# Kernel optimization log

Measured on AMD Instinct MI355X. Metric: run time of the kernel, lower is better.

The kernel has to match this reference:

```python
import jax, jax.numpy as jnp
import numpy as np

H = 256  # hidden_channels
N_USERS = 100000
N_MOVIES = 50000
N_EDGES = 500000


def setup_inputs() -> dict:
    key = jax.random.key(0)
    k1, k2, k3, k4, k5, k6, k7 = jax.random.split(key, 7)
    user_emb = jax.random.normal(k1, (N_USERS, H), dtype=jnp.float32)
    movie_emb = jax.random.normal(k2, (N_MOVIES, H), dtype=jnp.float32)
    edge_label_index = jax.random.randint(k3, (2, N_EDGES), 0, N_MOVIES, dtype=jnp.int64)
    # Linear(2H, H) and Linear(H, 1) params, torch default init scale
    s1 = 1.0 / np.sqrt(2 * H)
    s2 = 1.0 / np.sqrt(H)
    W1 = jax.random.uniform(k4, (2 * H, H), dtype=jnp.float32, minval=-s1, maxval=s1)
    b1 = jax.random.uniform(k5, (H,), dtype=jnp.float32, minval=-s1, maxval=s1)
    W2 = jax.random.uniform(k6, (H, 1), dtype=jnp.float32, minval=-s2, maxval=s2)
    b2 = jax.random.uniform(k7, (1,), dtype=jnp.float32, minval=-s2, maxval=s2)
    return {"user_emb": user_emb, "movie_emb": movie_emb,
            "edge_label_index": edge_label_index,
            "W1": W1, "b1": b1, "W2": W2, "b2": b2}


def reference(user_emb, movie_emb, edge_label_index, W1, b1, W2, b2):
    u = user_emb[edge_label_index[0]]    # [E, H]
    m = movie_emb[edge_label_index[1]]   # [E, H]
    x = jnp.concatenate([u, m], axis=-1)  # [E, 2H]
    x = jax.nn.relu(x @ W1 + b1)          # [E, H]
    return x @ W2 + b2                    # [E, 1]
```

## Files before the change

kernel.cpp:

```cpp
#include <hip/hip_runtime.h>
#include <hip/hip_bf16.h>

typedef __attribute__((ext_vector_type(8))) short v8s;
typedef __attribute__((ext_vector_type(4))) float v4f;

constexpr int H  = 256;
constexpr int K2 = 512;
constexpr int XS = 72;
constexpr int WS = 72;

__device__ inline unsigned short f2bf(float f) {
    unsigned int u = __builtin_bit_cast(unsigned int, f);
    u += 0x7FFFu + ((u >> 16) & 1u);
    return (unsigned short)(u >> 16);
}
__device__ inline float bf2f(unsigned short s) {
    return __builtin_bit_cast(float, (unsigned int)s << 16);
}

__global__ void w1_transpose_kernel(const float* __restrict__ w1,
                                    unsigned short* __restrict__ w1t) {
    __shared__ float tile[32][33];
    const int bk = blockIdx.x;
    const int bn = blockIdx.y;
    const int tx = threadIdx.x & 31;
    const int ty8 = threadIdx.x >> 5;
#pragma unroll
    for (int i = 0; i < 4; ++i) {
        int ty = i * 8 + ty8;
        tile[ty][tx] = w1[(size_t)(bk * 32 + ty) * H + bn * 32 + tx];
    }
    __syncthreads();
#pragma unroll
    for (int i = 0; i < 4; ++i) {
        int ty = i * 8 + ty8;
        w1t[(size_t)(bn * 32 + ty) * K2 + bk * 32 + tx] = f2bf(tile[tx][ty]);
    }
}

__global__ __launch_bounds__(512, 4) void emb_gemm_fused_kernel(
    const float* __restrict__ user_emb,
    const float* __restrict__ movie_emb,
    const unsigned short* __restrict__ w1t,
    const float* __restrict__ b1,
    unsigned short* __restrict__ P,
    unsigned short* __restrict__ Q,
    const int n_users, const int n_movies, const int nbu)
{
    __shared__ unsigned short Xs[64 * XS];
    __shared__ unsigned short Wts[H * WS];

    const int  isMovie = (blockIdx.x >= nbu) ? 1 : 0;
    const float* emb  = isMovie ? movie_emb : user_emb;
    unsigned short* outp = isMovie ? Q : P;
    const int  M     = isMovie ? n_movies : n_users;
    const int  kofs  = isMovie ? 256 : 0;
    const long m0    = (long)(blockIdx.x - (isMovie ? nbu : 0)) * 64;

    const int t    = threadIdx.x;
    const int wave = t >> 6;
    const int lane = t & 63;
    const int wm   = wave >> 2;
    const int wn   = wave & 3;
    const int quad = lane >> 4;
    const int l16  = lane & 15;

    const int xr = t >> 3;
    const int xc = t & 7;
    long mr = m0 + xr; if (mr >= M) mr = M - 1;
    const float* arow = emb + (size_t)mr * H;

    const int wr  = t >> 3;
    const int wc8 = t & 7;
    const unsigned short* wbase = w1t + (size_t)wr * K2 + kofs + wc8 * 8;

    v4f acc[2][4];
#pragma unroll
    for (int mt = 0; mt < 2; ++mt)
#pragma unroll
        for (int nt = 0; nt < 4; ++nt)
            acc[mt][nt] = (v4f){0.f, 0.f, 0.f, 0.f};

    v4f a0 = *(const v4f*)(arow + xc * 8);
    v4f a1 = *(const v4f*)(arow + xc * 8 + 4);
    v8s wq[4];
#pragma unroll
    for (int j = 0; j < 4; ++j)
        wq[j] = *(const v8s*)(wbase + (size_t)j * 64 * K2);

    for (int kt = 0; kt < 4; ++kt) {
        __syncthreads();
        {
            v8s xv;
#pragma unroll
            for (int i = 0; i < 4; ++i) { xv[i] = (short)f2bf(a0[i]); xv[4+i] = (short)f2bf(a1[i]); }
            *(v8s*)(Xs + xr * XS + xc * 8) = xv;
        }
#pragma unroll
        for (int j = 0; j < 4; ++j)
            *(v8s*)(Wts + (j * 64 + wr) * WS + wc8 * 8) = wq[j];
        if (kt < 3) {
            const int kn = kt + 1;
            a0 = *(const v4f*)(arow + kn * 64 + xc * 8);
            a1 = *(const v4f*)(arow + kn * 64 + xc * 8 + 4);
#pragma unroll
            for (int j = 0; j < 4; ++j)
                wq[j] = *(const v8s*)(wbase + (size_t)j * 64 * K2 + kn * 64);
        }
        __syncthreads();
#pragma unroll
        for (int ks = 0; ks < 2; ++ks) {
            v8s af[2], bf[4];
#pragma unroll
            for (int mt = 0; mt < 2; ++mt)
                af[mt] = *(const v8s*)(Xs + (wm * 32 + mt * 16 + l16) * XS + ks * 32 + quad * 8);
#pragma unroll
            for (int nt = 0; nt < 4; ++nt)
                bf[nt] = *(const v8s*)(Wts + (wn * 64 + nt * 16 + l16) * WS + ks * 32 + quad * 8);
#pragma unroll
            for (int mt = 0; mt < 2; ++mt)
#pragma unroll
                for (int nt = 0; nt < 4; ++nt)
                    acc[mt][nt] = __builtin_amdgcn_mfma_f32_16x16x32_bf16(
                        af[mt], bf[nt], acc[mt][nt], 0, 0, 0);
        }
    }

    float bv[4];
#pragma unroll
    for (int nt = 0; nt < 4; ++nt)
        bv[nt] = isMovie ? 0.f : b1[wn * 64 + nt * 16 + l16];

#pragma unroll
    for (int mt = 0; mt < 2; ++mt) {
#pragma unroll
        for (int j = 0; j < 4; ++j) {
            long m = m0 + wm * 32 + mt * 16 + quad * 4 + j;
            if (m < M) {
#pragma unroll
                for (int nt = 0; nt < 4; ++nt) {
                    int n = wn * 64 + nt * 16 + l16;
                    outp[(size_t)m * H + n] = f2bf(acc[mt][nt][j] + bv[nt]);
                }
            }
        }
    }
}

__global__ __launch_bounds__(256, 8) void edge_score_kernel(
    const unsigned short* __restrict__ P,
    const unsigned short* __restrict__ Q,
    const int* __restrict__ eli,
    const float* __restrict__ w2,
    const float* __restrict__ b2,
    float* __restrict__ out,
    const int E, const int n_users, const int n_movies)
{
    const int t   = threadIdx.x;
    const int hw  = t >> 5;
    const int l32 = t & 31;

    float w2v[8];
    {
        v4f a = *(const v4f*)(w2 + l32 * 8);
        v4f b = *(const v4f*)(w2 + l32 * 8 + 4);
#pragma unroll
        for (int i = 0; i < 4; ++i) { w2v[i] = a[i]; w2v[4 + i] = b[i]; }
    }
    const float b2v = b2[0];
    const long base = (long)blockIdx.x * 64;

    int us[8], ms[8];
#pragma unroll
    for (int i = 0; i < 8; ++i) {
        long e = base + i * 8 + hw;
        long ec = (e < E) ? e : 0;
        int u = eli[ec];
        int m = eli[(long)E + ec];
        us[i] = u < 0 ? 0 : (u >= n_users  ? n_users  - 1 : u);
        ms[i] = m < 0 ? 0 : (m >= n_movies ? n_movies - 1 : m);
    }

    v8s pv = *(const v8s*)(P + (size_t)us[0] * H + l32 * 8);
    v8s qv = *(const v8s*)(Q + (size_t)ms[0] * H + l32 * 8);

#pragma unroll
    for (int i = 0; i < 8; ++i) {
        v8s pn, qn;
        if (i < 7) {
            pn = *(const v8s*)(P + (size_t)us[i + 1] * H + l32 * 8);
            qn = *(const v8s*)(Q + (size_t)ms[i + 1] * H + l32 * 8);
        }
        float s = 0.f;
#pragma unroll
        for (int j = 0; j < 8; ++j) {
            float h = bf2f((unsigned short)pv[j]) + bf2f((unsigned short)qv[j]);
            h = h > 0.f ? h : 0.f;
            s += h * w2v[j];
        }
        s += __shfl_xor(s, 1, 64);
        s += __shfl_xor(s, 2, 64);
        s += __shfl_xor(s, 4, 64);
        s += __shfl_xor(s, 8, 64);
        s += __shfl_xor(s, 16, 64);
        long e = base + i * 8 + hw;
        if (l32 == 0 && e < E) out[e] = s + b2v;
        pv = pn; qv = qn;
    }
}

constexpr int BMF = 64;
__global__ __launch_bounds__(512, 4) void edge_decoder_kernel(
    const float* __restrict__ user_emb, const float* __restrict__ movie_emb,
    const int* __restrict__ eli, const unsigned short* __restrict__ w1t,
    const float* __restrict__ b1, const float* __restrict__ w2,
    const float* __restrict__ b2, float* __restrict__ out,
    const int E, const int n_users, const int n_movies)
{
    __shared__ unsigned short Xs[BMF * XS];
    __shared__ unsigned short Wts[H * WS];
    __shared__ float red[4][BMF];
    const int t = threadIdx.x, wave = t >> 6, lane = t & 63;
    const int wm = wave >> 2, wn = wave & 3, quad = lane >> 4, l16 = lane & 15;
    const long e0 = (long)blockIdx.x * BMF;
    const int xr = t >> 3, xc = t & 7;
    long eg = e0 + xr; if (eg >= E) eg = 0;
    int iu = eli[eg], im = eli[(long)E + eg];
    iu = iu < 0 ? 0 : (iu >= n_users ? n_users - 1 : iu);
    im = im < 0 ? 0 : (im >= n_movies ? n_movies - 1 : im);
    const float* urow = user_emb + (size_t)iu * H;
    const float* mrow = movie_emb + (size_t)im * H;
    const int wr = t >> 3, wc8 = t & 7;
    const unsigned short* wbase = w1t + (size_t)wr * K2 + wc8 * 8;
    v4f acc[2][4];
#pragma unroll
    for (int mt = 0; mt < 2; ++mt)
#pragma unroll
        for (int nt = 0; nt < 4; ++nt) acc[mt][nt] = (v4f){0.f,0.f,0.f,0.f};
    v4f xq0 = *(const v4f*)(urow + xc * 8);
    v4f xq1 = *(const v4f*)(urow + xc * 8 + 4);
    v8s wq[4];
#pragma unroll
    for (int j = 0; j < 4; ++j) wq[j] = *(const v8s*)(wbase + (size_t)j * 64 * K2);
    for (int kt = 0; kt < 8; ++kt) {
        __syncthreads();
        { v8s xv;
#pragma unroll
          for (int i = 0; i < 4; ++i) xv[i] = (short)f2bf(xq0[i]);
#pragma unroll
          for (int i = 0; i < 4; ++i) xv[4+i] = (short)f2bf(xq1[i]);
          *(v8s*)(Xs + xr * XS + xc * 8) = xv; }
#pragma unroll
        for (int j = 0; j < 4; ++j) *(v8s*)(Wts + (j * 64 + wr) * WS + wc8 * 8) = wq[j];
        if (kt < 7) {
            const int kn = kt + 1, koff = (kn * 64) & 255;
            const float* src = ((kn < 4) ? urow : mrow) + koff + xc * 8;
            xq0 = *(const v4f*)(src); xq1 = *(const v4f*)(src + 4);
#pragma unroll
            for (int j = 0; j < 4; ++j) wq[j] = *(const v8s*)(wbase + (size_t)j * 64 * K2 + kn * 64);
        }
        __syncthreads();
#pragma unroll
        for (int ks = 0; ks < 2; ++ks) {
            v8s af[2], bf[4];
#pragma unroll
            for (int mt = 0; mt < 2; ++mt)
                af[mt] = *(const v8s*)(Xs + (wm * 32 + mt * 16 + l16) * XS + ks * 32 + quad * 8);
#pragma unroll
            for (int nt = 0; nt < 4; ++nt)
                bf[nt] = *(const v8s*)(Wts + (wn * 64 + nt * 16 + l16) * WS + ks * 32 + quad * 8);
#pragma unroll
            for (int mt = 0; mt < 2; ++mt)
#pragma unroll
                for (int nt = 0; nt < 4; ++nt)
                    acc[mt][nt] = __builtin_amdgcn_mfma_f32_16x16x32_bf16(af[mt], bf[nt], acc[mt][nt], 0, 0, 0);
        }
    }
    float b1v[4], w2v[4];
#pragma unroll
    for (int nt = 0; nt < 4; ++nt) {
        int n = wn * 64 + nt * 16 + l16;
        b1v[nt] = b1[n]; w2v[nt] = w2[n];
    }
    const float b2v = b2[0];
#pragma unroll
    for (int mt = 0; mt < 2; ++mt) {
        float s[4] = {0.f,0.f,0.f,0.f};
#pragma unroll
        for (int nt = 0; nt < 4; ++nt)
#pragma unroll
            for (int j = 0; j < 4; ++j) {
                float h = acc[mt][nt][j] + b1v[nt];
                h = h > 0.f ? h : 0.f;
                s[j] += h * w2v[nt];
            }
#pragma unroll
        for (int j = 0; j < 4; ++j) {
            float v = s[j];
            v += __shfl_xor(v, 1, 64); v += __shfl_xor(v, 2, 64);
            v += __shfl_xor(v, 4, 64); v += __shfl_xor(v, 8, 64);
            if (l16 == 0) red[wn][wm * 32 + mt * 16 + quad * 4 + j] = v;
        }
    }
    __syncthreads();
    if (t < BMF) {
        long e = e0 + t;
        if (e < E) out[e] = red[0][t] + red[1][t] + red[2][t] + red[3][t] + b2v;
    }
}

extern "C" void kernel_launch(void* const* d_in, const int* in_sizes, int n_in,
                              void* d_out, int out_size, void* d_ws, size_t ws_size,
                              hipStream_t stream) {
    const float* user_emb  = (const float*)d_in[0];
    const float* movie_emb = (const float*)d_in[1];
    const int*   eli       = (const int*)d_in[2];
    const float* w1        = (const float*)d_in[3];
    const float* b1        = (const float*)d_in[4];
    const float* w2        = (const float*)d_in[5];
    const float* b2        = (const float*)d_in[6];
    float*       out       = (float*)d_out;

    const int E        = out_size;
    const int n_users  = in_sizes[0] / H;
    const int n_movies = in_sizes[1] / H;

    unsigned short* w1t = (unsigned short*)d_ws;
    const size_t w1t_bytes = (size_t)K2 * H * 2;
    const size_t p_bytes   = (size_t)n_users  * H * 2;
    const size_t q_bytes   = (size_t)n_movies * H * 2;

    w1_transpose_kernel<<<dim3(16, 8), 256, 0, stream>>>(w1, w1t);

    if (ws_size >= w1t_bytes + p_bytes + q_bytes) {
        unsigned short* P = (unsigned short*)((char*)d_ws + w1t_bytes);
        unsigned short* Q = (unsigned short*)((char*)d_ws + w1t_bytes + p_bytes);
        const int nbu = (n_users  + 63) / 64;
        const int nbm = (n_movies + 63) / 64;
        emb_gemm_fused_kernel<<<nbu + nbm, 512, 0, stream>>>(
            user_emb, movie_emb, w1t, b1, P, Q, n_users, n_movies, nbu);
        edge_score_kernel<<<(E + 63) / 64, 256, 0, stream>>>(
            P, Q, eli, w2, b2, out, E, n_users, n_movies);
    } else {
        edge_decoder_kernel<<<(E + BMF - 1) / BMF, 512, 0, stream>>>(
            user_emb, movie_emb, eli, w1t, b1, w2, b2, out, E, n_users, n_movies);
    }
}
```

Measured before the change: 286.9 us.

## Skip unreferenced embedding chunks and use persistent GEMM with register-resident weights

Two small kernels first zero and then fill per-64-row flags marking which user and movie chunks the edge indices actually reference. A persistent GEMM kernel replaces the one-block-per-tile version. Each block builds a list of active chunks with a ballot, keeps its W1 slice in registers, and stages bf16 X tiles in XOR-swizzled LDS while prefetching the next chunk. This cuts embedding reads and P/Q writes for rows no edge touches, at the cost of two extra launches and heavy register use with only 256 blocks.

```diff
diff --git a/kernel.cpp b/kernel.cpp
--- a/kernel.cpp
+++ b/kernel.cpp
@@ -17,6 +17,13 @@
 __device__ inline float bf2f(unsigned short s) {
     return __builtin_bit_cast(float, (unsigned int)s << 16);
 }
+
+#define BAR_LGKM() do {                                          \
+    asm volatile("s_waitcnt lgkmcnt(0)" ::: "memory");           \
+    __builtin_amdgcn_sched_barrier(0);                           \
+    __builtin_amdgcn_s_barrier();                                \
+    __builtin_amdgcn_sched_barrier(0);                           \
+} while (0)
 
 __global__ void w1_transpose_kernel(const float* __restrict__ w1,
                                     unsigned short* __restrict__ w1t) {
@@ -38,24 +45,53 @@
     }
 }
 
-__global__ __launch_bounds__(512, 4) void emb_gemm_fused_kernel(
+__global__ void flag_zero_kernel(unsigned char* __restrict__ f, const int n) {
+    int i = threadIdx.x + blockIdx.x * blockDim.x;
+    int stride = blockDim.x * gridDim.x;
+    for (; i < n; i += stride) f[i] = 0;
+}
+
+__global__ void flag_fill_kernel(const int* __restrict__ eli,
+                                 unsigned char* __restrict__ fu,
+                                 unsigned char* __restrict__ fm,
+                                 const int E, const int nu, const int nm) {
+    const long stride = (long)blockDim.x * gridDim.x;
+    for (long e = threadIdx.x + (long)blockIdx.x * blockDim.x; e < E; e += stride) {
+        int u = eli[e];
+        int m = eli[(long)E + e];
+        u = u < 0 ? 0 : (u >= nu ? nu - 1 : u);
+        m = m < 0 ? 0 : (m >= nm ? nm - 1 : m);
+        fu[u >> 6] = 1;
+        fm[m >> 6] = 1;
+    }
+}
+
+__global__ __launch_bounds__(512, 2) void emb_gemm_persist_kernel(
     const float* __restrict__ user_emb,
     const float* __restrict__ movie_emb,
     const unsigned short* __restrict__ w1t,
     const float* __restrict__ b1,
     unsigned short* __restrict__ P,
     unsigned short* __restrict__ Q,
-    const int n_users, const int n_movies, const int nbu)
+    const int n_users, const int n_movies,
+    const unsigned char* __restrict__ fu,
+    const unsigned char* __restrict__ fm)
 {
-    __shared__ unsigned short Xs[64 * XS];
-    __shared__ unsigned short Wts[H * WS];
-
-    const int  isMovie = (blockIdx.x >= nbu) ? 1 : 0;
-    const float* emb  = isMovie ? movie_emb : user_emb;
+    __shared__ __align__(16) unsigned short Xs[64 * 256];
+    __shared__ int list[64];
+    __shared__ int nact_s;
+
+    const int bid   = blockIdx.x;
+    const int nside = (int)(gridDim.x >> 1);
+    const int isMovie = bid & 1;
+    const int base  = bid >> 1;
+
+    const float* emb = isMovie ? movie_emb : user_emb;
     unsigned short* outp = isMovie ? Q : P;
-    const int  M     = isMovie ? n_movies : n_users;
-    const int  kofs  = isMovie ? 256 : 0;
-    const long m0    = (long)(blockIdx.x - (isMovie ? nbu : 0)) * 64;
+    const int M    = isMovie ? n_movies : n_users;
+    const int kofs = isMovie ? 256 : 0;
+    const int nch  = (M + 63) >> 6;
+    const unsigned char* flags = isMovie ? fm : fu;
 
     const int t    = threadIdx.x;
     const int wave = t >> 6;
@@ -65,84 +101,107 @@
     const int quad = lane >> 4;
     const int l16  = lane & 15;
 
-    const int xr = t >> 3;
-    const int xc = t & 7;
-    long mr = m0 + xr; if (mr >= M) mr = M - 1;
-    const float* arow = emb + (size_t)mr * H;
-
-    const int wr  = t >> 3;
-    const int wc8 = t & 7;
-    const unsigned short* wbase = w1t + (size_t)wr * K2 + kofs + wc8 * 8;
-
-    v4f acc[2][4];
-#pragma unroll
-    for (int mt = 0; mt < 2; ++mt)
+    if (wave == 0) {
+        int c = base + lane * nside;
+        bool a = (c < nch) && (flags[c] != 0);
+        unsigned long long mk = __ballot(a);
+        if (a) list[__popcll(mk & ((1ull << lane) - 1ull))] = c;
+        if (lane == 0) nact_s = (int)__popcll(mk);
+    }
+    __syncthreads();
+    const int nact = nact_s;
+    if (nact == 0) return;
+
+    v8s B[4][4][2];
+    {
+        const unsigned short* wb = w1t + (size_t)(wn * 64 + l16) * K2 + kofs + quad * 8;
 #pragma unroll
         for (int nt = 0; nt < 4; ++nt)
-            acc[mt][nt] = (v4f){0.f, 0.f, 0.f, 0.f};
-
-    v4f a0 = *(const v4f*)(arow + xc * 8);
-    v4f a1 = *(const v4f*)(arow + xc * 8 + 4);
-    v8s wq[4];
-#pragma unroll
-    for (int j = 0; j < 4; ++j)
-        wq[j] = *(const v8s*)(wbase + (size_t)j * 64 * K2);
-
-    for (int kt = 0; kt < 4; ++kt) {
-        __syncthreads();
-        {
-            v8s xv;
-#pragma unroll
-            for (int i = 0; i < 4; ++i) { xv[i] = (short)f2bf(a0[i]); xv[4+i] = (short)f2bf(a1[i]); }
-            *(v8s*)(Xs + xr * XS + xc * 8) = xv;
-        }
-#pragma unroll
-        for (int j = 0; j < 4; ++j)
-            *(v8s*)(Wts + (j * 64 + wr) * WS + wc8 * 8) = wq[j];
-        if (kt < 3) {
-            const int kn = kt + 1;
-            a0 = *(const v4f*)(arow + kn * 64 + xc * 8);
-            a1 = *(const v4f*)(arow + kn * 64 + xc * 8 + 4);
-#pragma unroll
-            for (int j = 0; j < 4; ++j)
-                wq[j] = *(const v8s*)(wbase + (size_t)j * 64 * K2 + kn * 64);
-        }
-        __syncthreads();
-#pragma unroll
-        for (int ks = 0; ks < 2; ++ks) {
-            v8s af[2], bf[4];
-#pragma unroll
-            for (int mt = 0; mt < 2; ++mt)
-                af[mt] = *(const v8s*)(Xs + (wm * 32 + mt * 16 + l16) * XS + ks * 32 + quad * 8);
-#pragma unroll
-            for (int nt = 0; nt < 4; ++nt)
-                bf[nt] = *(const v8s*)(Wts + (wn * 64 + nt * 16 + l16) * WS + ks * 32 + quad * 8);
-#pragma unroll
-            for (int mt = 0; mt < 2; ++mt)
-#pragma unroll
-                for (int nt = 0; nt < 4; ++nt)
-                    acc[mt][nt] = __builtin_amdgcn_mfma_f32_16x16x32_bf16(
-                        af[mt], bf[nt], acc[mt][nt], 0, 0, 0);
-        }
-    }
-
+#pragma unroll
+            for (int kt = 0; kt < 4; ++kt)
+#pragma unroll
+                for (int ks = 0; ks < 2; ++ks)
+                    B[nt][kt][ks] = *(const v8s*)(wb + (size_t)nt * 16 * K2 + kt * 64 + ks * 32);
+    }
     float bv[4];
 #pragma unroll
     for (int nt = 0; nt < 4; ++nt)
         bv[nt] = isMovie ? 0.f : b1[wn * 64 + nt * 16 + l16];
 
-#pragma unroll
-    for (int mt = 0; mt < 2; ++mt) {
-#pragma unroll
-        for (int j = 0; j < 4; ++j) {
-            long m = m0 + wm * 32 + mt * 16 + quad * 4 + j;
-            if (m < M) {
-#pragma unroll
-                for (int nt = 0; nt < 4; ++nt) {
-                    int n = wn * 64 + nt * 16 + l16;
-                    outp[(size_t)m * H + n] = f2bf(acc[mt][nt][j] + bv[nt]);
+    char* const xsb = (char*)Xs;
+    v4f xq[8];
+
+    auto LOADX = [&](int c) {
+#pragma unroll
+        for (int i = 0; i < 8; ++i) {
+            long r = (long)c * 64 + wave * 8 + i;
+            if (r >= M) r = M - 1;
+            xq[i] = *(const v4f*)(emb + (size_t)r * H + lane * 4);
+        }
+    };
+    auto WRITEX = [&]() {
+#pragma unroll
+        for (int i = 0; i < 8; ++i) {
+            const int r = wave * 8 + i;
+            unsigned int lo = (unsigned)f2bf(xq[i][0]) | ((unsigned)f2bf(xq[i][1]) << 16);
+            unsigned int hi = (unsigned)f2bf(xq[i][2]) | ((unsigned)f2bf(xq[i][3]) << 16);
+            *(unsigned long long*)(xsb + r * 512 + ((lane * 8) ^ (i << 4))) =
+                ((unsigned long long)hi << 32) | lo;
+        }
+    };
+
+    LOADX(list[0]);
+    WRITEX();
+    if (nact > 1) LOADX(list[1]);
+    __syncthreads();
+
+    for (int j = 0; j < nact; ++j) {
+        const long m0 = (long)list[j] * 64;
+
+        v4f acc[2][4];
+#pragma unroll
+        for (int mt = 0; mt < 2; ++mt)
+#pragma unroll
+            for (int nt = 0; nt < 4; ++nt)
+                acc[mt][nt] = (v4f){0.f, 0.f, 0.f, 0.f};
+
+#pragma unroll
+        for (int kt = 0; kt < 4; ++kt)
+#pragma unroll
+            for (int ks = 0; ks < 2; ++ks) {
+                v8s af[2];
+#pragma unroll
+                for (int mt = 0; mt < 2; ++mt) {
+                    const int row = wm * 32 + mt * 16 + l16;
+                    af[mt] = *(const v8s*)(xsb + row * 512 +
+                        ((kt * 128 + ks * 64 + quad * 16) ^ ((l16 & 7) << 4)));
+                }
+#pragma unroll
+                for (int mt = 0; mt < 2; ++mt)
+#pragma unroll
+                    for (int nt = 0; nt < 4; ++nt)
+                        acc[mt][nt] = __builtin_amdgcn_mfma_f32_16x16x32_bf16(
+                            af[mt], B[nt][kt][ks], acc[mt][nt], 0, 0, 0);
+            }
+
+#pragma unroll
+        for (int mt = 0; mt < 2; ++mt)
+#pragma unroll
+            for (int j4 = 0; j4 < 4; ++j4) {
+                const long m = m0 + wm * 32 + mt * 16 + quad * 4 + j4;
+                if (m < M) {
+#pragma unroll
+                    for (int nt = 0; nt < 4; ++nt)
+                        outp[(size_t)m * H + wn * 64 + nt * 16 + l16] =
+                            f2bf(acc[mt][nt][j4] + bv[nt]);
                 }
             }
+
+        if (j + 1 < nact) {
+            BAR_LGKM();
+            WRITEX();
+            if (j + 2 < nact) LOADX(list[j + 2]);
+            BAR_LGKM();
         }
     }
 }
@@ -330,19 +389,30 @@
     const size_t p_bytes   = (size_t)n_users  * H * 2;
     const size_t q_bytes   = (size_t)n_movies * H * 2;
 
+    const int nbu = (n_users  + 63) / 64;
+    const int nbm = (n_movies + 63) / 64;
+    const size_t flag_bytes = (size_t)nbu + (size_t)nbm;
+
     w1_transpose_kernel<<<dim3(16, 8), 256, 0, stream>>>(w1, w1t);
 
-    if (ws_size >= w1t_bytes + p_bytes + q_bytes) {
+    if (ws_size >= w1t_bytes + p_bytes + q_bytes + flag_bytes &&
+        nbu <= 64 * 128 && nbm <= 64 * 128) {
         unsigned short* P = (unsigned short*)((char*)d_ws + w1t_bytes);
         unsigned short* Q = (unsigned short*)((char*)d_ws + w1t_bytes + p_bytes);
-        const int nbu = (n_users  + 63) / 64;
-        const int nbm = (n_movies + 63) / 64;
-        emb_gemm_fused_kernel<<<nbu + nbm, 512, 0, stream>>>(
-            user_emb, movie_emb, w1t, b1, P, Q, n_users, n_movies, nbu);
-        edge_score_kernel<<<(E + 63) / 64, 256, 0, stream>>>(
-            P, Q, eli, w2, b2, out, E, n_users, n_movies);
+        unsigned char*  fu = (unsigned char*)((char*)d_ws + w1t_bytes + p_bytes + q_bytes);
+        unsigned char*  fm = fu + nbu;
+
+        flag_zero_kernel<<<4, 256, 0, stream>>>(fu, nbu + nbm);
+        if (E > 0)
+            flag_fill_kernel<<<512, 256, 0, stream>>>(eli, fu, fm, E, n_users, n_movies);
+        emb_gemm_persist_kernel<<<256, 512, 0, stream>>>(
+            user_emb, movie_emb, w1t, b1, P, Q, n_users, n_movies, fu, fm);
+        if (E > 0)
+            edge_score_kernel<<<(E + 63) / 64, 256, 0, stream>>>(
+                P, Q, eli, w2, b2, out, E, n_users, n_movies);
     } else {
-        edge_decoder_kernel<<<(E + BMF - 1) / BMF, 512, 0, stream>>>(
-            user_emb, movie_emb, eli, w1t, b1, w2, b2, out, E, n_users, n_movies);
-    }
-}
+        if (E > 0)
+            edge_decoder_kernel<<<(E + BMF - 1) / BMF, 512, 0, stream>>>(
+                user_emb, movie_emb, eli, w1t, b1, w2, b2, out, E, n_users, n_movies);
+    }
+}
```

New measurement: 263.7 us. 1.09x faster.
